# Optimization experiments

Hardware: AMD Instinct MI355X
Metric: run time of the kernel (lower is better)

Reference implementation:

```python
import jax, jax.numpy as jnp
import numpy as np

N_FFT = 256
WINDOW_OUT = 64
N_BINS = N_FFT // 2 + 1  # 129


def _irfft_matrices(n_fft, window_out):
    n = n_fft // 2 + 1
    m_real = np.fft.irfft(np.eye(n), n=n_fft)          # [n, n_fft]
    m_imag = np.fft.irfft(1j * np.eye(n), n=n_fft)     # [n, n_fft]
    m_real = m_real[:, -window_out:]                   # truncate to last window_out samples
    m_imag = m_imag[:, -window_out:]
    return (jnp.asarray(m_real, dtype=jnp.float32), jnp.asarray(m_imag, dtype=jnp.float32))


def setup_inputs() -> dict:
    key = jax.random.key(0)
    k1, k2 = jax.random.split(key)
    re = jax.random.normal(k1, (64, 4000, N_BINS), dtype=jnp.float32)
    im = jax.random.normal(k2, (64, 4000, N_BINS), dtype=jnp.float32)
    m_real, m_imag = _irfft_matrices(N_FFT, WINDOW_OUT)
    return {"re": re, "im": im, "m_real": m_real, "m_imag": m_imag}


def reference(re, im, m_real, m_imag):
    # Dense IRFFT: out = re @ M_real + im @ M_imag, fused add of the two matmul outputs.
    # re, im: [B, T, n_bins]; m_real, m_imag: [n_bins, window_out] -> out: [B, T, window_out]
    return jnp.einsum('btn,no->bto', re, m_real) + jnp.einsum('btn,no->bto', im, m_imag)
```

## Files before the change

kernel.cpp:

```cpp
#include <hip/hip_runtime.h>
#include <hip/hip_bf16.h>

typedef __bf16 bf8 __attribute__((ext_vector_type(8)));
typedef float f32x4 __attribute__((ext_vector_type(4)));
typedef unsigned short u16x4 __attribute__((ext_vector_type(4)));

#define NBINS 129
#define SROWS 64
#define KSTR 136
#define MATOFF (SROWS * KSTR)
#define SUBTILES 4

__device__ __forceinline__ unsigned short f2bf(float x) {
    return __builtin_bit_cast(unsigned short, (__bf16)x);
}

__global__ __launch_bounds__(256, 4)
void irfft_mm(const float* __restrict__ re,
              const float* __restrict__ im,
              const float* __restrict__ mr,
              const float* __restrict__ mi,
              float* __restrict__ out)
{
    __shared__ unsigned short lds[2 * MATOFF];

    const int tid  = threadIdx.x;
    const int lane = tid & 63;
    const int w    = tid >> 6;
    const int r16  = lane & 15;
    const int q    = lane >> 4;

    bf8 afr[2][4];
    #pragma unroll
    for (int m = 0; m < 2; ++m) {
        const float* M = m ? mi : mr;
        #pragma unroll
        for (int t = 0; t < 4; ++t) {
            bf8 v;
            #pragma unroll
            for (int j = 0; j < 8; ++j)
                v[j] = (__bf16)M[(t * 32 + q * 8 + j) * 64 + w * 16 + r16];
            afr[m][t] = v;
        }
    }
    const f32x4 mt0 = *(const f32x4*)(mr + 128 * 64 + w * 16 + q * 4);
    const f32x4 mt1 = *(const f32x4*)(mi + 128 * 64 + w * 16 + q * 4);

    for (int st = 0; st < SUBTILES; ++st) {
        const int rowbase = (blockIdx.x * SUBTILES + st) * SROWS;

        #pragma unroll
        for (int j = 0; j < 16; ++j) {
            const int F   = tid + j * 256;
            const int row = (F >> 5) & 63;
            const int c   = F & 31;
            const float* srcp = (j < 8) ? re : im;
            f32x4 v;
            __builtin_memcpy(&v, srcp + (rowbase + row) * NBINS + c * 4, 16);
            u16x4 h;
            h[0] = f2bf(v[0]); h[1] = f2bf(v[1]);
            h[2] = f2bf(v[2]); h[3] = f2bf(v[3]);
            *(u16x4*)&lds[(j >> 3) * MATOFF + row * KSTR + c * 4] = h;
        }
        if (tid < 128) {
            const float* srcp = (tid < 64) ? re : im;
            const int row = tid & 63;
            const float v = srcp[(rowbase + row) * NBINS + 128];
            lds[(tid >> 6) * MATOFF + row * KSTR + 128] = f2bf(v);
        }
        __syncthreads();

        f32x4 acc[4];
        #pragma unroll
        for (int rb = 0; rb < 4; ++rb) acc[rb] = {0.0f, 0.0f, 0.0f, 0.0f};

        #pragma unroll
        for (int m = 0; m < 2; ++m) {
            #pragma unroll
            for (int t = 0; t < 4; ++t) {
                bf8 bfr[4];
                #pragma unroll
                for (int rb = 0; rb < 4; ++rb)
                    bfr[rb] = *(const bf8*)&lds[m * MATOFF + (rb * 16 + r16) * KSTR
                                                + t * 32 + q * 8];
                #pragma unroll
                for (int rb = 0; rb < 4; ++rb)
                    acc[rb] = __builtin_amdgcn_mfma_f32_16x16x32_bf16(
                        afr[m][t], bfr[rb], acc[rb], 0, 0, 0);
            }
            const f32x4 mt = (m == 0) ? mt0 : mt1;
            #pragma unroll
            for (int rb = 0; rb < 4; ++rb) {
                const unsigned short h = lds[m * MATOFF + (rb * 16 + r16) * KSTR + 128];
                const float xt = (float)__builtin_bit_cast(__bf16, h);
                #pragma unroll
                for (int jj = 0; jj < 4; ++jj)
                    acc[rb][jj] += xt * mt[jj];
            }
        }
        __syncthreads();

        #pragma unroll
        for (int rb = 0; rb < 4; ++rb)
            *(f32x4*)(out + (rowbase + rb * 16 + r16) * 64 + w * 16 + q * 4) = acc[rb];
    }
}

extern "C" void kernel_launch(void* const* d_in, const int* in_sizes, int n_in,
                              void* d_out, int out_size, void* d_ws, size_t ws_size,
                              hipStream_t stream)
{
    const float* re = (const float*)d_in[0];
    const float* im = (const float*)d_in[1];
    const float* mr = (const float*)d_in[2];
    const float* mi = (const float*)d_in[3];
    float* out = (float*)d_out;

    const long rows = (long)in_sizes[0] / NBINS;
    const int grid = (int)(rows / (SUBTILES * SROWS));
    irfft_mm<<<grid, 256, 0, stream>>>(re, im, mr, mi, out);
}
```

Measured before the change: 75.44 us.

## Double-buffer LDS tiles and prefetch next tile's global loads into registers

Splits each block's work into 8 iterations of 32 rows, down from 4 subtiles of 64. The next tile's re/im loads are issued into registers before the current tile's MFMA work, and two LDS buffers alternate so only one barrier per iteration is needed. This aims to hide global load latency behind compute in this memory-bound kernel. The cost is more VGPRs for the prefetch buffer, with a risk of spilling or reduced occupancy under launch_bounds(256,4), and a manual barrier sequence that relies on double buffering for correctness.

```diff
diff --git a/kernel.cpp b/kernel.cpp
--- a/kernel.cpp
+++ b/kernel.cpp
@@ -6,13 +6,35 @@
 typedef unsigned short u16x4 __attribute__((ext_vector_type(4)));
 
 #define NBINS 129
-#define SROWS 64
+#define ROWS_IT 32
+#define ITERS 8
 #define KSTR 136
-#define MATOFF (SROWS * KSTR)
-#define SUBTILES 4
+#define MATOFF (ROWS_IT * KSTR)
+#define BUFE (2 * MATOFF)
 
 __device__ __forceinline__ unsigned short f2bf(float x) {
     return __builtin_bit_cast(unsigned short, (__bf16)x);
+}
+
+__device__ __forceinline__ void issue_loads(const float* __restrict__ re,
+                                            const float* __restrict__ im,
+                                            int rowbase, int tid,
+                                            f32x4* v, float* tl)
+{
+    #pragma unroll
+    for (int j = 0; j < 8; ++j) {
+        const int F = tid + j * 256;
+        const float* srcp = (j < 4) ? re : im;
+        const int row = (F >> 5) & 31;
+        const int c   = F & 31;
+        __builtin_memcpy(&v[j], srcp + (long)(rowbase + row) * NBINS + c * 4, 16);
+    }
+    float t = 0.0f;
+    if (tid < 64) {
+        const float* srcp = (tid < 32) ? re : im;
+        t = srcp[(long)(rowbase + (tid & 31)) * NBINS + 128];
+    }
+    *tl = t;
 }
 
 __global__ __launch_bounds__(256, 4)
@@ -22,7 +44,7 @@
               const float* __restrict__ mi,
               float* __restrict__ out)
 {
-    __shared__ unsigned short lds[2 * MATOFF];
+    __shared__ unsigned short lds[2][BUFE];
 
     const int tid  = threadIdx.x;
     const int lane = tid & 63;
@@ -30,79 +52,79 @@
     const int r16  = lane & 15;
     const int q    = lane >> 4;
 
+    const int blockrow = blockIdx.x * (ROWS_IT * ITERS);
+
+    f32x4 v[8]; float tl;
+    issue_loads(re, im, blockrow, tid, v, &tl);
+
     bf8 afr[2][4];
     #pragma unroll
     for (int m = 0; m < 2; ++m) {
         const float* M = m ? mi : mr;
         #pragma unroll
         for (int t = 0; t < 4; ++t) {
-            bf8 v;
+            bf8 a;
             #pragma unroll
             for (int j = 0; j < 8; ++j)
-                v[j] = (__bf16)M[(t * 32 + q * 8 + j) * 64 + w * 16 + r16];
-            afr[m][t] = v;
+                a[j] = (__bf16)M[(t * 32 + q * 8 + j) * 64 + w * 16 + r16];
+            afr[m][t] = a;
         }
     }
     const f32x4 mt0 = *(const f32x4*)(mr + 128 * 64 + w * 16 + q * 4);
     const f32x4 mt1 = *(const f32x4*)(mi + 128 * 64 + w * 16 + q * 4);
 
-    for (int st = 0; st < SUBTILES; ++st) {
-        const int rowbase = (blockIdx.x * SUBTILES + st) * SROWS;
+    for (int it = 0; it < ITERS; ++it) {
+        unsigned short* buf = lds[it & 1];
+        const int rowbase = blockrow + it * ROWS_IT;
 
         #pragma unroll
-        for (int j = 0; j < 16; ++j) {
+        for (int j = 0; j < 8; ++j) {
             const int F   = tid + j * 256;
-            const int row = (F >> 5) & 63;
+            const int mat = j >> 2;
+            const int row = (F >> 5) & 31;
             const int c   = F & 31;
-            const float* srcp = (j < 8) ? re : im;
-            f32x4 v;
-            __builtin_memcpy(&v, srcp + (rowbase + row) * NBINS + c * 4, 16);
             u16x4 h;
-            h[0] = f2bf(v[0]); h[1] = f2bf(v[1]);
-            h[2] = f2bf(v[2]); h[3] = f2bf(v[3]);
-            *(u16x4*)&lds[(j >> 3) * MATOFF + row * KSTR + c * 4] = h;
+            h[0] = f2bf(v[j][0]); h[1] = f2bf(v[j][1]);
+            h[2] = f2bf(v[j][2]); h[3] = f2bf(v[j][3]);
+            *(u16x4*)&buf[mat * MATOFF + row * KSTR + c * 4] = h;
         }
-        if (tid < 128) {
-            const float* srcp = (tid < 64) ? re : im;
-            const int row = tid & 63;
-            const float v = srcp[(rowbase + row) * NBINS + 128];
-            lds[(tid >> 6) * MATOFF + row * KSTR + 128] = f2bf(v);
-        }
-        __syncthreads();
+        if (tid < 64)
+            buf[(tid >> 5) * MATOFF + (tid & 31) * KSTR + 128] = f2bf(tl);
 
-        f32x4 acc[4];
-        #pragma unroll
-        for (int rb = 0; rb < 4; ++rb) acc[rb] = {0.0f, 0.0f, 0.0f, 0.0f};
+        if (it + 1 < ITERS)
+            issue_loads(re, im, rowbase + ROWS_IT, tid, v, &tl);
+
+        asm volatile("s_waitcnt lgkmcnt(0)" ::: "memory");
+        __builtin_amdgcn_s_barrier();
+        asm volatile("" ::: "memory");
+
+        f32x4 acc[2];
+        acc[0] = {0.0f, 0.0f, 0.0f, 0.0f};
+        acc[1] = {0.0f, 0.0f, 0.0f, 0.0f};
 
         #pragma unroll
         for (int m = 0; m < 2; ++m) {
             #pragma unroll
             for (int t = 0; t < 4; ++t) {
-                bf8 bfr[4];
-                #pragma unroll
-                for (int rb = 0; rb < 4; ++rb)
-                    bfr[rb] = *(const bf8*)&lds[m * MATOFF + (rb * 16 + r16) * KSTR
-                                                + t * 32 + q * 8];
-                #pragma unroll
-                for (int rb = 0; rb < 4; ++rb)
-                    acc[rb] = __builtin_amdgcn_mfma_f32_16x16x32_bf16(
-                        afr[m][t], bfr[rb], acc[rb], 0, 0, 0);
+                bf8 b0 = *(const bf8*)&buf[m * MATOFF + r16 * KSTR + t * 32 + q * 8];
+                bf8 b1 = *(const bf8*)&buf[m * MATOFF + (16 + r16) * KSTR + t * 32 + q * 8];
+                acc[0] = __builtin_amdgcn_mfma_f32_16x16x32_bf16(afr[m][t], b0, acc[0], 0, 0, 0);
+                acc[1] = __builtin_amdgcn_mfma_f32_16x16x32_bf16(afr[m][t], b1, acc[1], 0, 0, 0);
             }
-            const f32x4 mt = (m == 0) ? mt0 : mt1;
+            const f32x4 mt = m ? mt1 : mt0;
             #pragma unroll
-            for (int rb = 0; rb < 4; ++rb) {
-                const unsigned short h = lds[m * MATOFF + (rb * 16 + r16) * KSTR + 128];
+            for (int rb = 0; rb < 2; ++rb) {
+                const unsigned short h = buf[m * MATOFF + (rb * 16 + r16) * KSTR + 128];
                 const float xt = (float)__builtin_bit_cast(__bf16, h);
                 #pragma unroll
                 for (int jj = 0; jj < 4; ++jj)
                     acc[rb][jj] += xt * mt[jj];
             }
         }
-        __syncthreads();
 
         #pragma unroll
-        for (int rb = 0; rb < 4; ++rb)
-            *(f32x4*)(out + (rowbase + rb * 16 + r16) * 64 + w * 16 + q * 4) = acc[rb];
+        for (int rb = 0; rb < 2; ++rb)
+            *(f32x4*)(out + (long)(rowbase + rb * 16 + r16) * 64 + w * 16 + q * 4) = acc[rb];
     }
 }
 
@@ -117,6 +139,6 @@
     float* out = (float*)d_out;
 
     const long rows = (long)in_sizes[0] / NBINS;
-    const int grid = (int)(rows / (SUBTILES * SROWS));
+    const int grid = (int)(rows / (ROWS_IT * ITERS));
     irfft_mm<<<grid, 256, 0, stream>>>(re, im, mr, mi, out);
 }
```

Result: faster. 67.87 us (-10.0%).

## Stream inputs directly into registers with prefetch instead of LDS staging

Applied to the files above, without the earlier changes.

Inputs are no longer staged through LDS. Each wave loads its 16-row strip of re/im straight from global memory into registers, converts to bf16 there, and feeds the MFMA, with a register double buffer that prefetches the next half-tile. The transform matrices are transposed once per block into LDS to build the A fragments, and blocks now cover 128 rows over 8 iterations, which doubles the grid. This removes the LDS round trip and the block-wide barriers. In exchange, all four waves read the same input rows, which multiplies L1/L2 traffic, and every block reloads the 64KB matrix.

```diff
diff --git a/kernel.cpp b/kernel.cpp
--- a/kernel.cpp
+++ b/kernel.cpp
@@ -3,13 +3,12 @@
 
 typedef __bf16 bf8 __attribute__((ext_vector_type(8)));
 typedef float f32x4 __attribute__((ext_vector_type(4)));
-typedef unsigned short u16x4 __attribute__((ext_vector_type(4)));
 
 #define NBINS 129
-#define SROWS 64
+#define ROWB 516
+#define ITERS 8
 #define KSTR 136
-#define MATOFF (SROWS * KSTR)
-#define SUBTILES 4
+#define MATOFF (64 * KSTR)
 
 __device__ __forceinline__ unsigned short f2bf(float x) {
     return __builtin_bit_cast(unsigned short, (__bf16)x);
@@ -22,7 +21,7 @@
               const float* __restrict__ mi,
               float* __restrict__ out)
 {
-    __shared__ unsigned short lds[2 * MATOFF];
+    __shared__ unsigned short mt[2 * MATOFF];
 
     const int tid  = threadIdx.x;
     const int lane = tid & 63;
@@ -30,79 +29,94 @@
     const int r16  = lane & 15;
     const int q    = lane >> 4;
 
+    for (int e = tid; e < 128 * 64; e += 256) {
+        const int k = e >> 6, c = e & 63;
+        mt[c * KSTR + k]          = f2bf(mr[e]);
+        mt[MATOFF + c * KSTR + k] = f2bf(mi[e]);
+    }
+    __syncthreads();
+
     bf8 afr[2][4];
     #pragma unroll
+    for (int m = 0; m < 2; ++m)
+        #pragma unroll
+        for (int t = 0; t < 4; ++t)
+            afr[m][t] = *(const bf8*)&mt[m * MATOFF + (w * 16 + r16) * KSTR
+                                         + t * 32 + q * 8];
+    const f32x4 mtr = *(const f32x4*)(mr + 128 * 64 + w * 16 + q * 4);
+    const f32x4 mti = *(const f32x4*)(mi + 128 * 64 + w * 16 + q * 4);
+
+    const long blockrow = (long)blockIdx.x * (ITERS * 16);
+    const char* prer = (const char*)re + (blockrow + r16) * (long)ROWB;
+    const char* prei = (const char*)im + (blockrow + r16) * (long)ROWB;
+    float* pout = out + (blockrow + r16) * 64 + w * 16 + q * 4;
+
+    f32x4 vf[2][2][2];
+    float trr[2], tri[2];
+
+    #pragma unroll
     for (int m = 0; m < 2; ++m) {
-        const float* M = m ? mi : mr;
+        const char* sp = m ? prei : prer;
         #pragma unroll
-        for (int t = 0; t < 4; ++t) {
-            bf8 v;
+        for (int t2 = 0; t2 < 2; ++t2)
             #pragma unroll
-            for (int j = 0; j < 8; ++j)
-                v[j] = (__bf16)M[(t * 32 + q * 8 + j) * 64 + w * 16 + r16];
-            afr[m][t] = v;
+            for (int p2 = 0; p2 < 2; ++p2)
+                __builtin_memcpy(&vf[m][t2][p2], sp + t2 * 128 + q * 32 + p2 * 16, 16);
+    }
+    trr[0] = *(const float*)(prer + 512);
+    tri[0] = *(const float*)(prei + 512);
+
+    f32x4 acc = {0.f, 0.f, 0.f, 0.f};
+
+    #pragma unroll
+    for (int p = 0; p < 2 * ITERS; ++p) {
+        const int it = p >> 1, h = p & 1;
+
+        bf8 bfr[2][2];
+        #pragma unroll
+        for (int m = 0; m < 2; ++m)
+            #pragma unroll
+            for (int t2 = 0; t2 < 2; ++t2)
+                #pragma unroll
+                for (int j = 0; j < 4; ++j) {
+                    bfr[m][t2][j]     = (__bf16)vf[m][t2][0][j];
+                    bfr[m][t2][4 + j] = (__bf16)vf[m][t2][1][j];
+                }
+
+        if (p + 1 < 2 * ITERS) {
+            const int itn = (p + 1) >> 1, hn = (p + 1) & 1;
+            const long ro = (long)itn * (16 * ROWB) + hn * 256;
+            #pragma unroll
+            for (int m = 0; m < 2; ++m) {
+                const char* sp = m ? prei : prer;
+                #pragma unroll
+                for (int t2 = 0; t2 < 2; ++t2)
+                    #pragma unroll
+                    for (int p2 = 0; p2 < 2; ++p2)
+                        __builtin_memcpy(&vf[m][t2][p2],
+                                         sp + ro + t2 * 128 + q * 32 + p2 * 16, 16);
+            }
+            if (hn == 0) {
+                trr[itn & 1] = *(const float*)(prer + (long)itn * (16 * ROWB) + 512);
+                tri[itn & 1] = *(const float*)(prei + (long)itn * (16 * ROWB) + 512);
+            }
         }
-    }
-    const f32x4 mt0 = *(const f32x4*)(mr + 128 * 64 + w * 16 + q * 4);
-    const f32x4 mt1 = *(const f32x4*)(mi + 128 * 64 + w * 16 + q * 4);
-
-    for (int st = 0; st < SUBTILES; ++st) {
-        const int rowbase = (blockIdx.x * SUBTILES + st) * SROWS;
 
         #pragma unroll
-        for (int j = 0; j < 16; ++j) {
-            const int F   = tid + j * 256;
-            const int row = (F >> 5) & 63;
-            const int c   = F & 31;
-            const float* srcp = (j < 8) ? re : im;
-            f32x4 v;
-            __builtin_memcpy(&v, srcp + (rowbase + row) * NBINS + c * 4, 16);
-            u16x4 h;
-            h[0] = f2bf(v[0]); h[1] = f2bf(v[1]);
-            h[2] = f2bf(v[2]); h[3] = f2bf(v[3]);
-            *(u16x4*)&lds[(j >> 3) * MATOFF + row * KSTR + c * 4] = h;
+        for (int m = 0; m < 2; ++m)
+            #pragma unroll
+            for (int t2 = 0; t2 < 2; ++t2)
+                acc = __builtin_amdgcn_mfma_f32_16x16x32_bf16(
+                    afr[m][h * 2 + t2], bfr[m][t2], acc, 0, 0, 0);
+
+        if (h) {
+            const float xr = trr[it & 1], xi = tri[it & 1];
+            #pragma unroll
+            for (int jj = 0; jj < 4; ++jj)
+                acc[jj] += xr * mtr[jj] + xi * mti[jj];
+            *(f32x4*)(pout + (long)it * 1024) = acc;
+            acc = (f32x4){0.f, 0.f, 0.f, 0.f};
         }
-        if (tid < 128) {
-            const float* srcp = (tid < 64) ? re : im;
-            const int row = tid & 63;
-            const float v = srcp[(rowbase + row) * NBINS + 128];
-            lds[(tid >> 6) * MATOFF + row * KSTR + 128] = f2bf(v);
-        }
-        __syncthreads();
-
-        f32x4 acc[4];
-        #pragma unroll
-        for (int rb = 0; rb < 4; ++rb) acc[rb] = {0.0f, 0.0f, 0.0f, 0.0f};
-
-        #pragma unroll
-        for (int m = 0; m < 2; ++m) {
-            #pragma unroll
-            for (int t = 0; t < 4; ++t) {
-                bf8 bfr[4];
-                #pragma unroll
-                for (int rb = 0; rb < 4; ++rb)
-                    bfr[rb] = *(const bf8*)&lds[m * MATOFF + (rb * 16 + r16) * KSTR
-                                                + t * 32 + q * 8];
-                #pragma unroll
-                for (int rb = 0; rb < 4; ++rb)
-                    acc[rb] = __builtin_amdgcn_mfma_f32_16x16x32_bf16(
-                        afr[m][t], bfr[rb], acc[rb], 0, 0, 0);
-            }
-            const f32x4 mt = (m == 0) ? mt0 : mt1;
-            #pragma unroll
-            for (int rb = 0; rb < 4; ++rb) {
-                const unsigned short h = lds[m * MATOFF + (rb * 16 + r16) * KSTR + 128];
-                const float xt = (float)__builtin_bit_cast(__bf16, h);
-                #pragma unroll
-                for (int jj = 0; jj < 4; ++jj)
-                    acc[rb][jj] += xt * mt[jj];
-            }
-        }
-        __syncthreads();
-
-        #pragma unroll
-        for (int rb = 0; rb < 4; ++rb)
-            *(f32x4*)(out + (rowbase + rb * 16 + r16) * 64 + w * 16 + q * 4) = acc[rb];
     }
 }
 
@@ -117,6 +131,6 @@
     float* out = (float*)d_out;
 
     const long rows = (long)in_sizes[0] / NBINS;
-    const int grid = (int)(rows / (SUBTILES * SROWS));
+    const int grid = (int)(rows / (ITERS * 16));
     irfft_mm<<<grid, 256, 0, stream>>>(re, im, mr, mi, out);
 }
```

Result: slower. 175.9 us (+133.1%).
